# Kernel optimization log

Hardware: AMD Instinct MI355X
Metric: run time of the kernel (lower is better)

Reference implementation:

```python
import jax, jax.numpy as jnp
import numpy as np

BATCH_SIZE = 4096
N_VIEWS = 2
NUM_GPU = 1
TEMPERATURE = 0.07
FEAT_DIM = 128
N = (BATCH_SIZE // NUM_GPU) * N_VIEWS  # 8192


def setup_inputs() -> dict:
    key = jax.random.key(0)
    features = jax.random.normal(key, (N, FEAT_DIM), dtype=jnp.float32)
    return {"features": features}


def reference(features):
    n = features.shape[0]
    b = BATCH_SIZE // NUM_GPU
    # labels: [arange(b)] * n_views concatenated -> pairwise equality matrix
    lbl_vec = jnp.tile(jnp.arange(b), N_VIEWS)            # [N]
    lab = lbl_vec[None, :] == lbl_vec[:, None]            # [N, N] bool

    # F.normalize(dim=1): divide by L2 norm clamped at 1e-12
    norm = jnp.linalg.norm(features, axis=1, keepdims=True)
    f = features / jnp.maximum(norm, 1e-12)
    sim = f @ f.T                                          # [N, N]

    # Remove diagonal: row i keeps columns j != i in original order.
    cols = jnp.arange(n - 1)
    off_idx = cols[None, :] + (cols[None, :] >= jnp.arange(n)[:, None])  # [N, N-1]
    sim_od = jnp.take_along_axis(sim, off_idx, axis=1)     # [N, N-1]
    lab_od = jnp.take_along_axis(lab, off_idx, axis=1)     # [N, N-1] bool

    # Stable sort: positives (label True) first, preserving original column order,
    # matching torch's masked-select + concat([positives, negatives]).
    order = jnp.argsort(~lab_od, axis=1, stable=True)      # [N, N-1]
    logits = jnp.take_along_axis(sim_od, order, axis=1) / TEMPERATURE

    # CrossEntropyLoss with target class 0 (mean reduction)
    loss = -jax.nn.log_softmax(logits, axis=1)[:, 0]
    return loss.mean()
```

## Files before the change

kernel.cpp:

```cpp
#include <hip/hip_runtime.h>
#include <hip/hip_bf16.h>
#include <cstdint>

#define NROWS 8192
#define FDIM  128
#define HALF_N 4096

typedef short bf16x8 __attribute__((ext_vector_type(8)));
typedef float f32x4  __attribute__((ext_vector_type(4)));

#define K1 (1.4426950408889634f / 0.07f)

#if __has_builtin(__builtin_amdgcn_exp2f)
#define EXP2(x) __builtin_amdgcn_exp2f(x)
#else
#define EXP2(x) exp2f(x)
#endif


__global__ void __launch_bounds__(256) normalize_kernel(const float* __restrict__ f,
                                                        short* __restrict__ packed,
                                                        float* __restrict__ esum_g) {
    const int row  = blockIdx.x * 4 + (threadIdx.x >> 6);
    const int lane = threadIdx.x & 63;
    const float2 v = ((const float2*)(f + (size_t)row * FDIM))[lane];
    float ss = v.x * v.x + v.y * v.y;
    #pragma unroll
    for (int m = 1; m < 64; m <<= 1) ss += __shfl_xor(ss, m);
    const float scale = 1.0f / fmaxf(sqrtf(ss), 1e-12f);

    const int off = ((((row >> 4) * 4 + (lane >> 4)) * 64)
                     + ((lane >> 2) & 3) * 16 + (row & 15)) * 8 + 2 * (lane & 3);
    __hip_bfloat16 b0 = __float2bfloat16(v.x * scale);
    __hip_bfloat16 b1 = __float2bfloat16(v.y * scale);
    unsigned u = (unsigned)*(unsigned short*)&b0
               | ((unsigned)*(unsigned short*)&b1 << 16);
    *(unsigned*)(packed + off) = u;

    if (threadIdx.x < 4) esum_g[blockIdx.x * 4 + threadIdx.x] = 0.0f;
}

__device__ __forceinline__ float2 bf2_to_f2(unsigned u) {
    return make_float2(__uint_as_float(u << 16),
                       __uint_as_float(u & 0xffff0000u));
}

__global__ void __launch_bounds__(256, 2) sim_kernel(const short* __restrict__ pk,
                                                     float* __restrict__ esum_g,
                                                     float* __restrict__ pos_g,
                                                     float* __restrict__ diag_g) {
    if (blockIdx.x >= 512) {
        const int i  = (blockIdx.x - 512) * 256 + threadIdx.x;
        const int ip = i ^ HALF_N;
        const uint4* P = (const uint4*)pk;
        float dot = 0.f, self = 0.f;
        #pragma unroll
        for (int cc = 0; cc < 16; cc++) {
            const uint4 a = P[((i  >> 4) * 4 + (cc >> 2)) * 64 + (cc & 3) * 16 + (i  & 15)];
            const uint4 b = P[((ip >> 4) * 4 + (cc >> 2)) * 64 + (cc & 3) * 16 + (ip & 15)];
            const unsigned au[4] = {a.x, a.y, a.z, a.w};
            const unsigned bu[4] = {b.x, b.y, b.z, b.w};
            #pragma unroll
            for (int q = 0; q < 4; q++) {
                const float2 av = bf2_to_f2(au[q]);
                const float2 bv = bf2_to_f2(bu[q]);
                dot  = __builtin_fmaf(av.x, bv.x, __builtin_fmaf(av.y, bv.y, dot));
                self = __builtin_fmaf(av.x, av.x, __builtin_fmaf(av.y, av.y, self));
            }
        }
        pos_g[i]  = dot;
        diag_g[i] = EXP2(__builtin_fmaf(self, K1, -K1));
        return;
    }

    const int tid   = threadIdx.x;
    const int w     = tid >> 6;
    const int lane  = tid & 63;
    const int quad  = lane >> 4;
    const int l16   = lane & 15;
    const int strip = blockIdx.x >> 2;
    const int c     = (blockIdx.x & 3) * 4 + w;
    const bf16x8* P = (const bf16x8*)pk;

    bf16x8 a_reg[4][4];
    #pragma unroll
    for (int fr = 0; fr < 4; fr++)
        #pragma unroll
        for (int ks = 0; ks < 4; ks++)
            a_reg[ks][fr] = P[((strip * 4 + fr) * 4 + ks) * 64 + lane];

    float ep[4][4];
    #pragma unroll
    for (int a = 0; a < 4; a++)
        #pragma unroll
        for (int b = 0; b < 4; b++) ep[a][b] = 0.0f;

    auto cb_clamp = [&](int p) { return (p < 260) ? p : c; };
    auto cb_base  = [&](int p) {
        const int d = p >> 2, fc = p & 3;
        const int js = (strip + d) & 127;
        return ((js * 4 + fc) * 4) * 64 + lane;
    };

    bf16x8 bbuf[3][4];
    {
        const int b0 = cb_base(cb_clamp(c));
        const int b1 = cb_base(cb_clamp(c + 16));
        #pragma unroll
        for (int ks = 0; ks < 4; ks++) {
            bbuf[0][ks] = P[b0 + ks * 64];
            bbuf[1][ks] = P[b1 + ks * 64];
        }
    }

    #pragma unroll
    for (int k = 0; k < 17; k++) {
        if (k + 2 < 17) {
            const int bn = cb_base(cb_clamp(c + 16 * (k + 2)));
            #pragma unroll
            for (int ks = 0; ks < 4; ks++)
                bbuf[(k + 2) % 3][ks] = P[bn + ks * 64];
        }
        const int p = c + 16 * k;
        if (p < 260) {
            const int d  = p >> 2, fc = p & 3;
            const int js = (strip + d) & 127;

            f32x4 acc[4];
            #pragma unroll
            for (int fr = 0; fr < 4; fr++) acc[fr] = (f32x4){0.f, 0.f, 0.f, 0.f};
            #pragma unroll
            for (int ks = 0; ks < 4; ks++)
                #pragma unroll
                for (int fr = 0; fr < 4; fr++)
                    acc[fr] = __builtin_amdgcn_mfma_f32_16x16x32_bf16(
                                  a_reg[ks][fr], bbuf[k % 3][ks], acc[fr], 0, 0, 0);

            float cs = 0.0f;
            #pragma unroll
            for (int fr = 0; fr < 4; fr++)
                #pragma unroll
                for (int r = 0; r < 4; r++) {
                    const float e = EXP2(__builtin_fmaf(acc[fr][r], K1, -K1));
                    ep[fr][r] += e;
                    cs += e;
                }
            if (d != 0 && d != 64) {
                cs += __shfl_xor(cs, 16);
                cs += __shfl_xor(cs, 32);
                if (lane < 16)
                    atomicAdd(&esum_g[js * 64 + fc * 16 + lane], cs);
            }
        }
    }

    #pragma unroll
    for (int fr = 0; fr < 4; fr++)
        #pragma unroll
        for (int r = 0; r < 4; r++) {
            float v = ep[fr][r];
            #pragma unroll
            for (int m = 1; m < 16; m <<= 1) v += __shfl_xor(v, m);
            if (l16 == 0)
                atomicAdd(&esum_g[strip * 64 + fr * 16 + quad * 4 + r], v);
        }
}

__global__ void __launch_bounds__(256) final_kernel(const float* __restrict__ esum_g,
                                                    const float* __restrict__ pos_g,
                                                    const float* __restrict__ diag_g,
                                                    float* __restrict__ out) {
    const int tid = threadIdx.x;
    const float invT = 1.0f / 0.07f;
    float acc = 0.0f;
    for (int i = tid; i < NROWS; i += 256)
        acc += logf(esum_g[i] - diag_g[i]) + invT - pos_g[i] * invT;
    #pragma unroll
    for (int m = 1; m < 64; m <<= 1) acc += __shfl_xor(acc, m);
    __shared__ float ws[4];
    if ((tid & 63) == 0) ws[tid >> 6] = acc;
    __syncthreads();
    if (tid == 0) out[0] = (ws[0] + ws[1] + ws[2] + ws[3]) * (1.0f / (float)NROWS);
}

extern "C" void kernel_launch(void* const* d_in, const int* in_sizes, int n_in,
                              void* d_out, int out_size, void* d_ws, size_t ws_size,
                              hipStream_t stream) {
    const float* features = (const float*)d_in[0];
    float* out = (float*)d_out;

    char* ws = (char*)d_ws;
    short* packed = (short*)ws;
    float* esum_g = (float*)(ws + (size_t)NROWS * FDIM * 2);
    float* pos_g  = (float*)(ws + (size_t)NROWS * FDIM * 2 + NROWS * 4);
    float* diag_g = (float*)(ws + (size_t)NROWS * FDIM * 2 + NROWS * 8);

    normalize_kernel<<<NROWS / 4, 256, 0, stream>>>(features, packed, esum_g);

    sim_kernel<<<512 + NROWS / 256, 256, 0, stream>>>(packed, esum_g, pos_g, diag_g);

    final_kernel<<<1, 256, 0, stream>>>(esum_g, pos_g, diag_g, out);
}
```

Measured before the change: 107.3 us.

## Replace column atomics with per-tile buffer and parallelize final reduction

After: 111.3 us. 3.7% more time.

```diff
diff --git a/kernel.cpp b/kernel.cpp
--- a/kernel.cpp
+++ b/kernel.cpp
@@ -20,7 +20,8 @@
 
 __global__ void __launch_bounds__(256) normalize_kernel(const float* __restrict__ f,
                                                         short* __restrict__ packed,
-                                                        float* __restrict__ esum_g) {
+                                                        float* __restrict__ esum_g,
+                                                        float* __restrict__ out) {
     const int row  = blockIdx.x * 4 + (threadIdx.x >> 6);
     const int lane = threadIdx.x & 63;
     const float2 v = ((const float2*)(f + (size_t)row * FDIM))[lane];
@@ -38,6 +39,7 @@
     *(unsigned*)(packed + off) = u;
 
     if (threadIdx.x < 4) esum_g[blockIdx.x * 4 + threadIdx.x] = 0.0f;
+    if (blockIdx.x == 0 && threadIdx.x == 4) out[0] = 0.0f;
 }
 
 __device__ __forceinline__ float2 bf2_to_f2(unsigned u) {
@@ -45,12 +47,13 @@
                        __uint_as_float(u & 0xffff0000u));
 }
 
-__global__ void __launch_bounds__(256, 2) sim_kernel(const short* __restrict__ pk,
+__global__ void __launch_bounds__(256, 3) sim_kernel(const short* __restrict__ pk,
                                                      float* __restrict__ esum_g,
                                                      float* __restrict__ pos_g,
-                                                     float* __restrict__ diag_g) {
-    if (blockIdx.x >= 512) {
-        const int i  = (blockIdx.x - 512) * 256 + threadIdx.x;
+                                                     float* __restrict__ diag_g,
+                                                     float* __restrict__ colsc) {
+    if (blockIdx.x >= 768) {
+        const int i  = (blockIdx.x - 768) * 256 + threadIdx.x;
         const int ip = i ^ HALF_N;
         const uint4* P = (const uint4*)pk;
         float dot = 0.f, self = 0.f;
@@ -78,8 +81,8 @@
     const int lane  = tid & 63;
     const int quad  = lane >> 4;
     const int l16   = lane & 15;
-    const int strip = blockIdx.x >> 2;
-    const int c     = (blockIdx.x & 3) * 4 + w;
+    const int strip = blockIdx.x / 6;
+    const int c     = (blockIdx.x % 6) * 4 + w;
     const bf16x8* P = (const bf16x8*)pk;
 
     bf16x8 a_reg[4][4];
@@ -95,33 +98,29 @@
         #pragma unroll
         for (int b = 0; b < 4; b++) ep[a][b] = 0.0f;
 
-    auto cb_clamp = [&](int p) { return (p < 260) ? p : c; };
-    auto cb_base  = [&](int p) {
+    auto cb_base = [&](int p) {
         const int d = p >> 2, fc = p & 3;
         const int js = (strip + d) & 127;
         return ((js * 4 + fc) * 4) * 64 + lane;
     };
 
-    bf16x8 bbuf[3][4];
+    bf16x8 bb[2][4];
     {
-        const int b0 = cb_base(cb_clamp(c));
-        const int b1 = cb_base(cb_clamp(c + 16));
-        #pragma unroll
-        for (int ks = 0; ks < 4; ks++) {
-            bbuf[0][ks] = P[b0 + ks * 64];
-            bbuf[1][ks] = P[b1 + ks * 64];
-        }
+        const int b0 = cb_base(c);
+        #pragma unroll
+        for (int ks = 0; ks < 4; ks++) bb[0][ks] = P[b0 + ks * 64];
     }
 
     #pragma unroll
-    for (int k = 0; k < 17; k++) {
-        if (k + 2 < 17) {
-            const int bn = cb_base(cb_clamp(c + 16 * (k + 2)));
+    for (int k = 0; k < 11; k++) {
+        if (k < 10) {
+            const int pn = c + 24 * (k + 1);
+            const int bn = cb_base(pn < 260 ? pn : c);
             #pragma unroll
             for (int ks = 0; ks < 4; ks++)
-                bbuf[(k + 2) % 3][ks] = P[bn + ks * 64];
-        }
-        const int p = c + 16 * k;
+                bb[(k + 1) & 1][ks] = P[bn + ks * 64];
+        }
+        const int p = c + 24 * k;
         if (p < 260) {
             const int d  = p >> 2, fc = p & 3;
             const int js = (strip + d) & 127;
@@ -134,7 +133,7 @@
                 #pragma unroll
                 for (int fr = 0; fr < 4; fr++)
                     acc[fr] = __builtin_amdgcn_mfma_f32_16x16x32_bf16(
-                                  a_reg[ks][fr], bbuf[k % 3][ks], acc[fr], 0, 0, 0);
+                                  a_reg[ks][fr], bb[k & 1][ks], acc[fr], 0, 0, 0);
 
             float cs = 0.0f;
             #pragma unroll
@@ -149,7 +148,7 @@
                 cs += __shfl_xor(cs, 16);
                 cs += __shfl_xor(cs, 32);
                 if (lane < 16)
-                    atomicAdd(&esum_g[js * 64 + fc * 16 + lane], cs);
+                    colsc[((d - 1) * 128 + strip) * 64 + fc * 16 + lane] = cs;
             }
         }
     }
@@ -166,21 +165,26 @@
         }
 }
 
-__global__ void __launch_bounds__(256) final_kernel(const float* __restrict__ esum_g,
-                                                    const float* __restrict__ pos_g,
-                                                    const float* __restrict__ diag_g,
-                                                    float* __restrict__ out) {
-    const int tid = threadIdx.x;
+__global__ void __launch_bounds__(256) reduce_kernel(const float* __restrict__ esum_g,
+                                                     const float* __restrict__ pos_g,
+                                                     const float* __restrict__ diag_g,
+                                                     const float* __restrict__ colsc,
+                                                     float* __restrict__ out) {
+    const int j   = blockIdx.x * 256 + threadIdx.x;
+    const int js  = j >> 6, c64 = j & 63;
+    float cs = 0.0f;
+    #pragma unroll 7
+    for (int d = 1; d <= 63; d++)
+        cs += colsc[((d - 1) * 128 + ((js - d) & 127)) * 64 + c64];
     const float invT = 1.0f / 0.07f;
-    float acc = 0.0f;
-    for (int i = tid; i < NROWS; i += 256)
-        acc += logf(esum_g[i] - diag_g[i]) + invT - pos_g[i] * invT;
-    #pragma unroll
-    for (int m = 1; m < 64; m <<= 1) acc += __shfl_xor(acc, m);
-    __shared__ float ws[4];
-    if ((tid & 63) == 0) ws[tid >> 6] = acc;
+    float loss = logf(esum_g[j] + cs - diag_g[j]) + invT - pos_g[j] * invT;
+    #pragma unroll
+    for (int m = 1; m < 64; m <<= 1) loss += __shfl_xor(loss, m);
+    __shared__ float wsm[4];
+    if ((threadIdx.x & 63) == 0) wsm[threadIdx.x >> 6] = loss;
     __syncthreads();
-    if (tid == 0) out[0] = (ws[0] + ws[1] + ws[2] + ws[3]) * (1.0f / (float)NROWS);
+    if (threadIdx.x == 0)
+        atomicAdd(out, (wsm[0] + wsm[1] + wsm[2] + wsm[3]) * (1.0f / (float)NROWS));
 }
 
 extern "C" void kernel_launch(void* const* d_in, const int* in_sizes, int n_in,
@@ -191,13 +195,15 @@
 
     char* ws = (char*)d_ws;
     short* packed = (short*)ws;
-    float* esum_g = (float*)(ws + (size_t)NROWS * FDIM * 2);
-    float* pos_g  = (float*)(ws + (size_t)NROWS * FDIM * 2 + NROWS * 4);
-    float* diag_g = (float*)(ws + (size_t)NROWS * FDIM * 2 + NROWS * 8);
-
-    normalize_kernel<<<NROWS / 4, 256, 0, stream>>>(features, packed, esum_g);
-
-    sim_kernel<<<512 + NROWS / 256, 256, 0, stream>>>(packed, esum_g, pos_g, diag_g);
-
-    final_kernel<<<1, 256, 0, stream>>>(esum_g, pos_g, diag_g, out);
-}
+    float* esum_g = (float*)(ws + 2097152);
+    float* pos_g  = (float*)(ws + 2097152 + 32768);
+    float* diag_g = (float*)(ws + 2097152 + 65536);
+    float* colsc  = (float*)(ws + 2097152 + 98304);
+
+    normalize_kernel<<<NROWS / 4, 256, 0, stream>>>(features, packed, esum_g, out);
+
+    sim_kernel<<<768 + NROWS / 256, 256, 0, stream>>>(packed, esum_g, pos_g,
+                                                      diag_g, colsc);
+
+    reduce_kernel<<<NROWS / 256, 256, 0, stream>>>(esum_g, pos_g, diag_g, colsc, out);
+}
```
